# Kernel optimization log

Measured on AMD Instinct MI355X. Metric: run time of the kernel, lower is better.

The kernel has to match this reference:

```python
import jax, jax.numpy as jnp
import numpy as np

DT = 0.001  # fixed dt in SimplifiedSSM.forward
LN_EPS = 1e-5


def _layernorm(x, g, b):
    m = jnp.mean(x, axis=-1, keepdims=True)
    v = jnp.mean(jnp.square(x - m), axis=-1, keepdims=True)
    return (x - m) * jax.lax.rsqrt(v + LN_EPS) * g + b


def setup_inputs() -> dict:
    key = jax.random.key(0)
    ks = jax.random.split(key, 12)
    Bn, C, H, W = 8, 1024, 32, 32
    depth, S = 4, 128
    d = C
    inp = {
        "x": jax.random.normal(ks[0], (Bn, C, H, W), dtype=jnp.float32),
        # SSM params, stacked over depth. A scaled by 0.1 for numerical stability
        # of the length-1024 recurrence (same math, tamer eigenvalues).
        "A": 0.1 * jax.random.normal(ks[1], (depth, S, S), dtype=jnp.float32),
        "Bp": jax.random.normal(ks[2], (depth, S, d), dtype=jnp.float32),
        "Cp": jax.random.normal(ks[3], (depth, d, S), dtype=jnp.float32),
        "Dp": jax.random.normal(ks[4], (depth, d), dtype=jnp.float32),
        # Linear layers (PyTorch convention: y = x @ W.T + b)
        "Wi": jax.random.normal(ks[5], (depth, d, d), dtype=jnp.float32) / np.sqrt(d),
        "bi": jax.random.normal(ks[6], (depth, d), dtype=jnp.float32) * 0.01,
        "Wo": jax.random.normal(ks[7], (depth, d, d), dtype=jnp.float32) / np.sqrt(d),
        "bo": jax.random.normal(ks[8], (depth, d), dtype=jnp.float32) * 0.01,
        # LayerNorm affine params
        "gamma": jnp.ones((depth, d), dtype=jnp.float32),
        "beta": jnp.zeros((depth, d), dtype=jnp.float32),
    }
    return inp


def reference(x, A, Bp, Cp, Dp, Wi, bi, Wo, bo, gamma, beta):
    Bn, C, H, W = x.shape
    depth, S, _ = A.shape
    # b c h w -> b (h w) c
    seq = x.reshape(Bn, C, H * W).transpose(0, 2, 1)
    eye = jnp.eye(S, dtype=x.dtype)
    for i in range(depth):
        n = _layernorm(seq, gamma[i], beta[i])
        u = n @ Wi[i].T + bi[i]                       # (B, L, d)
        A_bar = eye + DT * A[i]                       # (S, S)
        ub = jnp.einsum('bld,sd->lbs', u, DT * Bp[i]) # (L, B, S)

        def step(h, ub_t):
            h = h @ A_bar.T + ub_t
            return h, h

        h0 = jnp.zeros((Bn, S), dtype=x.dtype)
        _, hs = jax.lax.scan(step, h0, ub)            # hs: (L, B, S)
        y = jnp.einsum('lbs,ds->bld', hs, Cp[i]) + u * Dp[i]
        seq = seq + y @ Wo[i].T + bo[i]
    return seq.transpose(0, 2, 1).reshape(Bn, C, H, W)
```

## Files before the change

kernel.cpp:

```cpp
#include <hip/hip_runtime.h>
#include <stdint.h>

#define DT_STEP 0.001f
#define LN_EPS  1e-5f
#define Bn      8
#define Lseq    1024
#define Dm      1024
#define Sn      128
#define DEPTH   4
#define Mrows   (Bn * Lseq)
#define Qc      32
#define NCHUNK  (Lseq / Qc)
#define NPOW    33

typedef short bf16x8 __attribute__((ext_vector_type(8)));
typedef float f32x4  __attribute__((ext_vector_type(4)));

__device__ __forceinline__ unsigned short f2bf(float f) {
    unsigned int u = __float_as_uint(f);
    u += 0x7fffu + ((u >> 16) & 1u);
    return (unsigned short)(u >> 16);
}

#define GLOAD_LDS16(gp, lp)                                                \
    __builtin_amdgcn_global_load_lds(                                      \
        (const __attribute__((address_space(1))) unsigned int*)(gp),       \
        (__attribute__((address_space(3))) unsigned int*)(lp), 16, 0, 0)

__global__ __launch_bounds__(256) void prep_conv(const float* __restrict__ Wo,
                                                 const float* __restrict__ Dp,
                                                 const float* __restrict__ Bp,
                                                 const float* __restrict__ bi,
                                                 const float* __restrict__ bo,
                                                 unsigned short* __restrict__ Woh,
                                                 unsigned short* __restrict__ Wo2h,
                                                 unsigned short* __restrict__ Bph,
                                                 float* __restrict__ c2dt,
                                                 float* __restrict__ boeff) {
    int z = blockIdx.y;
    int bx = blockIdx.x;
    int tid = threadIdx.x;
    if (bx < 1024) {
        int i = (bx * 256 + tid) * 4;
        const float* S = Wo + (size_t)z * Dm * Dm;
        float4 v = *(const float4*)(S + i);
        int c = i & (Dm - 1);
        float4 d = *(const float4*)(Dp + (size_t)z * Dm + c);
        ushort4 o1, o2;
        o1.x = f2bf(v.x); o1.y = f2bf(v.y); o1.z = f2bf(v.z); o1.w = f2bf(v.w);
        o2.x = f2bf(v.x * d.x); o2.y = f2bf(v.y * d.y);
        o2.z = f2bf(v.z * d.z); o2.w = f2bf(v.w * d.w);
        *(ushort4*)(Woh  + (size_t)z * Dm * Dm + i) = o1;
        *(ushort4*)(Wo2h + (size_t)z * Dm * Dm + i) = o2;
        return;
    } else if (bx < 1152) {
        int i = ((bx - 1024) * 256 + tid) * 4;
        float4 v = *(const float4*)(Bp + (size_t)z * Sn * Dm + i);
        ushort4 o;
        o.x = f2bf(v.x); o.y = f2bf(v.y); o.z = f2bf(v.z); o.w = f2bf(v.w);
        *(ushort4*)(Bph + (size_t)z * Sn * Dm + i) = o;
        return;
    }
    int j = bx - 1152;
    float acc;
    if (j < Sn) {
        const float* br = Bp + ((size_t)z * Sn + j) * Dm;
        const float* bb = bi + (size_t)z * Dm;
        float4 v = *(const float4*)(br + tid * 4);
        float4 w = *(const float4*)(bb + tid * 4);
        acc = v.x * w.x + v.y * w.y + v.z * w.z + v.w * w.w;
    } else {
        int c = j - Sn;
        const float* wr = Wo + ((size_t)z * Dm + c) * Dm;
        const float* dp = Dp + (size_t)z * Dm;
        const float* bb = bi + (size_t)z * Dm;
        float4 w = *(const float4*)(wr + tid * 4);
        float4 d = *(const float4*)(dp + tid * 4);
        float4 b = *(const float4*)(bb + tid * 4);
        acc = w.x * d.x * b.x + w.y * d.y * b.y + w.z * d.z * b.z + w.w * d.w * b.w;
    }
#pragma unroll
    for (int off = 32; off > 0; off >>= 1) acc += __shfl_down(acc, off, 64);
    __shared__ float red[4];
    if ((tid & 63) == 0) red[tid >> 6] = acc;
    __syncthreads();
    if (tid == 0) {
        float tot = red[0] + red[1] + red[2] + red[3];
        if (j < Sn) c2dt[z * Sn + j] = DT_STEP * tot;
        else        boeff[(size_t)z * Dm + (j - Sn)] = bo[(size_t)z * Dm + (j - Sn)] + tot;
    }
}

__global__ __launch_bounds__(256) void transpose_pre(const float* __restrict__ Wi,
                                                     unsigned short* __restrict__ WiTh,
                                                     const float* __restrict__ Cp,
                                                     unsigned short* __restrict__ CpTh) {
    __shared__ float t[32][33];
    int z = blockIdx.z;
    const float* S;
    unsigned short* D;
    int R, C, r0, c0;
    if ((int)blockIdx.x < 32) {
        S = Wi + (size_t)z * Dm * Dm;  D = WiTh + (size_t)z * Dm * Dm;
        R = Dm; C = Dm;
        r0 = blockIdx.y * 32; c0 = blockIdx.x * 32;
    } else {
        S = Cp + (size_t)z * Dm * Sn;  D = CpTh + (size_t)z * Dm * Sn;
        R = Dm; C = Sn;
        r0 = blockIdx.y * 32; c0 = (blockIdx.x - 32) * 32;
    }
    int tx = threadIdx.x & 31, ty = threadIdx.x >> 5;
    for (int rr = ty; rr < 32; rr += 8)
        t[rr][tx] = S[(size_t)(r0 + rr) * C + c0 + tx];
    __syncthreads();
    for (int rr = ty; rr < 32; rr += 8)
        D[(size_t)(c0 + rr) * R + r0 + tx] = f2bf(t[tx][rr]);
}

__global__ __launch_bounds__(1024) void transpose_bll(const float* __restrict__ src,
                                                      float* __restrict__ dst) {
    __shared__ float tile[32][33];
    int b  = blockIdx.z;
    int i0 = blockIdx.y * 32, j0 = blockIdx.x * 32;
    int tx = threadIdx.x, ty = threadIdx.y;
    const float* S = src + (size_t)b * Dm * Lseq;
    float*       D = dst + (size_t)b * Dm * Lseq;
    tile[ty][tx] = S[(size_t)(j0 + ty) * 1024 + i0 + tx];
    __syncthreads();
    D[(size_t)(i0 + ty) * 1024 + j0 + tx] = tile[tx][ty];
}

__global__ __launch_bounds__(512) void ln_ub(
    const float* __restrict__ seq,
    unsigned short* __restrict__ nbuf,
    const unsigned short* __restrict__ M2,
    float* __restrict__ ub,
    const float* __restrict__ gam,
    const float* __restrict__ bet,
    const float* __restrict__ c2dtL) {
    __shared__ __align__(16) unsigned short As[256 * 8];
    __shared__ __align__(16) unsigned short Bs[1024 * 8];
    __shared__ float mrow[32], rrow[32];
    int row0 = blockIdx.x * 32;
    int tid = threadIdx.x;

    {
        int r = tid >> 4, l = tid & 15;
        const float* xr = seq + (size_t)(row0 + r) * Dm + l * 4;
        float s = 0.f, ss = 0.f;
#pragma unroll
        for (int j = 0; j < 16; j++) {
            float4 v = *(const float4*)(xr + j * 64);
            s  += v.x + v.y + v.z + v.w;
            ss += v.x * v.x + v.y * v.y + v.z * v.z + v.w * v.w;
        }
        s += __shfl_xor(s, 1, 16);  ss += __shfl_xor(ss, 1, 16);
        s += __shfl_xor(s, 2, 16);  ss += __shfl_xor(ss, 2, 16);
        s += __shfl_xor(s, 4, 16);  ss += __shfl_xor(ss, 4, 16);
        s += __shfl_xor(s, 8, 16);  ss += __shfl_xor(ss, 8, 16);
        if (l == 0) {
            float mean = s / (float)Dm;
            float var  = ss / (float)Dm - mean * mean;
            mrow[r] = mean;
            rrow[r] = rsqrtf(var + LN_EPS);
        }
    }
    __syncthreads();
#pragma unroll
    for (int g = 0; g < 8; g++) {
        int gi = tid + g * 512;
        int rA = gi >> 7, gc = gi & 127;
        int col = gc * 8;
        const float* p = seq + (size_t)(row0 + rA) * Dm + col;
        float4 v0 = *(const float4*)(p);
        float4 v1 = *(const float4*)(p + 4);
        float m = mrow[rA], rs = rrow[rA];
        float4 g0 = *(const float4*)(gam + col);
        float4 g1 = *(const float4*)(gam + col + 4);
        float4 b0 = *(const float4*)(bet + col);
        float4 b1 = *(const float4*)(bet + col + 4);
        bf16x8 pk;
        pk[0] = (short)f2bf((v0.x - m) * rs * g0.x + b0.x);
        pk[1] = (short)f2bf((v0.y - m) * rs * g0.y + b0.y);
        pk[2] = (short)f2bf((v0.z - m) * rs * g0.z + b0.z);
        pk[3] = (short)f2bf((v0.w - m) * rs * g0.w + b0.w);
        pk[4] = (short)f2bf((v1.x - m) * rs * g1.x + b1.x);
        pk[5] = (short)f2bf((v1.y - m) * rs * g1.y + b1.y);
        pk[6] = (short)f2bf((v1.z - m) * rs * g1.z + b1.z);
        pk[7] = (short)f2bf((v1.w - m) * rs * g1.w + b1.w);
        *(bf16x8*)(nbuf + (size_t)(row0 + rA) * Dm + col) = pk;
    }
    __syncthreads();

    int wave = tid >> 6, lane = tid & 63;
    int wn = wave * 16;
    int lr = lane & 15, lq = lane >> 4;

    int rowA = tid >> 3;
    int kclA = (tid & 7) ^ ((tid >> 3) & 7);
    int rowS[2], kclS[2], slotOff[2];
#pragma unroll
    for (int q = 0; q < 2; q++) {
        int s = tid + q * 512;
        rowS[q] = s >> 3;
        kclS[q] = (s & 7) ^ ((s >> 3) & 7);
        slotOff[q] = s * 8;
    }
    int aoff[2][2], boff[2];
#pragma unroll
    for (int i = 0; i < 2; i++)
#pragma unroll
        for (int h = 0; h < 2; h++) {
            int ra = i * 16 + lr;
            aoff[i][h] = (ra * 8 + ((lq + 4 * h) ^ (ra & 7))) * 8;
        }
#pragma unroll
    for (int h = 0; h < 2; h++) {
        int rn = wn + lr;
        boff[h] = (rn * 8 + ((lq + 4 * h) ^ (rn & 7))) * 8;
    }

    f32x4 acc[2];
#pragma unroll
    for (int i = 0; i < 2; i++) acc[i] = (f32x4){0.f, 0.f, 0.f, 0.f};

    for (int k0 = 0; k0 < Dm; k0 += 64) {
        const unsigned short* Abr = nbuf + (size_t)row0 * Dm + k0;
        const unsigned short* Bbr = M2 + k0;
        __syncthreads();
        if (tid < 256)
            GLOAD_LDS16(Abr + (size_t)rowA * Dm + kclA * 8, &As[tid * 8]);
#pragma unroll
        for (int q = 0; q < 2; q++)
            GLOAD_LDS16(Bbr + (size_t)rowS[q] * Dm + kclS[q] * 8, &Bs[slotOff[q]]);
        __syncthreads();
#pragma unroll
        for (int h = 0; h < 2; h++) {
            bf16x8 af[2], bfr;
#pragma unroll
            for (int i = 0; i < 2; i++) af[i] = *(const bf16x8*)&As[aoff[i][h]];
            bfr = *(const bf16x8*)&Bs[boff[h]];
#pragma unroll
            for (int i = 0; i < 2; i++)
                acc[i] = __builtin_amdgcn_mfma_f32_16x16x32_bf16(af[i], bfr,
                                                                 acc[i], 0, 0, 0);
        }
    }
#pragma unroll
    for (int i = 0; i < 2; i++)
#pragma unroll
        for (int r = 0; r < 4; r++) {
            int row = row0 + i * 16 + lq * 4 + r;
            int col = wn + lr;
            ub[(size_t)row * Sn + col] = acc[i][r] + c2dtL[col];
        }
}

__device__ __forceinline__ void gemm64_body(
    int flat, unsigned short* As, unsigned short* Bs,
    const unsigned short* __restrict__ A, const unsigned short* __restrict__ B,
    float* __restrict__ C, const float* __restrict__ bias, int K) {
    int rb = flat & 63, cb = flat >> 6;
    int row0 = rb * 128, col0 = cb * 64;
    int tid  = threadIdx.x;
    int wave = tid >> 6, lane = tid & 63;
    int wm = (wave & 1) * 64, wn = (wave >> 1) * 16;
    int lr = lane & 15, lq = lane >> 4;

    int rowS[2], kclS[2], slotOff[2];
#pragma unroll
    for (int q = 0; q < 2; q++) {
        int s = tid + q * 512;
        rowS[q] = s >> 3;
        kclS[q] = (s & 7) ^ ((s >> 3) & 7);
        slotOff[q] = s * 8;
    }
    int rowB = tid >> 3;
    int kclB = (tid & 7) ^ ((tid >> 3) & 7);

    int aoff[4][2], boff[2];
#pragma unroll
    for (int i = 0; i < 4; i++)
#pragma unroll
        for (int h = 0; h < 2; h++) {
            int ra = wm + i * 16 + lr;
            aoff[i][h] = (ra * 8 + ((lq + 4 * h) ^ (ra & 7))) * 8;
        }
#pragma unroll
    for (int h = 0; h < 2; h++) {
        int rn = wn + lr;
        boff[h] = (rn * 8 + ((lq + 4 * h) ^ (rn & 7))) * 8;
    }

    f32x4 acc[4];
#pragma unroll
    for (int i = 0; i < 4; i++) acc[i] = (f32x4){0.f, 0.f, 0.f, 0.f};

    for (int k0 = 0; k0 < K; k0 += 64) {
        const unsigned short* Abr = A + (size_t)row0 * K + k0;
        const unsigned short* Bbr = B + (size_t)col0 * K + k0;
        __syncthreads();
#pragma unroll
        for (int q = 0; q < 2; q++)
            GLOAD_LDS16(Abr + (size_t)rowS[q] * K + kclS[q] * 8, &As[slotOff[q]]);
        GLOAD_LDS16(Bbr + (size_t)rowB * K + kclB * 8, &Bs[tid * 8]);
        __syncthreads();
#pragma unroll
        for (int h = 0; h < 2; h++) {
            bf16x8 af[4], bf;
#pragma unroll
            for (int i = 0; i < 4; i++) af[i] = *(const bf16x8*)&As[aoff[i][h]];
            bf = *(const bf16x8*)&Bs[boff[h]];
#pragma unroll
            for (int i = 0; i < 4; i++)
                acc[i] = __builtin_amdgcn_mfma_f32_16x16x32_bf16(af[i], bf,
                                                                 acc[i], 0, 0, 0);
        }
    }
#pragma unroll
    for (int i = 0; i < 4; i++)
#pragma unroll
        for (int r = 0; r < 4; r++) {
            int row = row0 + wm + i * 16 + lq * 4 + r;
            int col = col0 + wn + lr;
            size_t idx = (size_t)row * Dm + col;
            float v = acc[i][r];
            if (bias) v += bias[col];
            C[idx] = C[idx] + v;
        }
}

__global__ __launch_bounds__(512) void mega2(
    int mode,
    const unsigned short* __restrict__ nbuf,
    const unsigned short* __restrict__ W4,
    float* __restrict__ seq,
    const float* __restrict__ boeff,
    const float* __restrict__ ub,
    float* __restrict__ hs,
    unsigned short* __restrict__ hs_bf,
    const float* __restrict__ PowL,
    float* __restrict__ carryb) {
    __shared__ __align__(16) char smem[33280];
    int tid = threadIdx.x;
    int bid = blockIdx.x;

    bool isSerial;
    int sid, gflat;
    if (mode == 0)      { isSerial = (bid & 1) == 0; sid = bid >> 1; gflat = bid >> 1; }
    else if (mode == 1) { int q = bid / 33, r = bid % 33;
                          isSerial = (r == 0); sid = q; gflat = 256 + q * 32 + r - 1; }
    else                { int q = bid / 3, r = bid % 3;
                          isSerial = (r == 0); sid = q; gflat = 512 + q * 2 + (r - 1); }

    if (!isSerial) {
        unsigned short* As = (unsigned short*)smem;
        unsigned short* Bs = (unsigned short*)(smem + 16384);
        gemm64_body(gflat, As, Bs, nbuf, W4, seq, boeff, Dm);
        return;
    }

    __builtin_amdgcn_s_setprio(1);

    if (mode == 0) {
        float* hsh = (float*)smem;
        float* hp  = hsh + 128;
        int b = sid >> 5, c = sid & 31;
        int s = tid & 127, kq = tid >> 7;
        const float* Abar = PowL + (size_t)Sn * Sn;
        float arow[32];
#pragma unroll
        for (int j = 0; j < 32; j += 4) {
            float4 v = *(const float4*)(Abar + (size_t)s * Sn + kq * 32 + j);
            arow[j] = v.x; arow[j + 1] = v.y; arow[j + 2] = v.z; arow[j + 3] = v.w;
        }
        if (tid < 128) hsh[tid] = 0.f;
        __syncthreads();
        size_t base = (size_t)(b * Lseq + c * Qc) * Sn + s;
        float ut = (kq == 0) ? ub[base] : 0.f;
        const float* hq = &hsh[kq * 32];
        for (int t = 0; t < Qc; t++) {
            float utn = (kq == 0 && t + 1 < Qc) ? ub[base + (size_t)(t + 1) * Sn] : 0.f;
            float a0 = 0.f, a1 = 0.f, a2 = 0.f, a3 = 0.f;
#pragma unroll
            for (int j = 0; j < 32; j += 16) {
                float4 h0 = *(const float4*)&hq[j];
                float4 h1 = *(const float4*)&hq[j + 4];
                float4 h2 = *(const float4*)&hq[j + 8];
                float4 h3 = *(const float4*)&hq[j + 12];
                a0 += arow[j + 0] * h0.x + arow[j + 1] * h0.y + arow[j + 2] * h0.z + arow[j + 3] * h0.w;
                a1 += arow[j + 4] * h1.x + arow[j + 5] * h1.y + arow[j + 6] * h1.z + arow[j + 7] * h1.w;
                a2 += arow[j + 8] * h2.x + arow[j + 9] * h2.y + arow[j + 10] * h2.z + arow[j + 11] * h2.w;
                a3 += arow[j + 12] * h3.x + arow[j + 13] * h3.y + arow[j + 14] * h3.z + arow[j + 15] * h3.w;
            }
            hp[kq * 128 + s] = (a0 + a1) + (a2 + a3);
            __syncthreads();
            if (kq == 0) {
                float hv = ut + (hp[s] + hp[128 + s]) + (hp[256 + s] + hp[384 + s]);
                hs[base + (size_t)t * Sn] = hv;
                hsh[s] = hv;
            }
            __syncthreads();
            ut = utn;
        }
    } else if (mode == 1) {
        float* csh = (float*)smem;
        float* cp  = csh + 128;
        int b = sid;
        int s = tid & 127, kq = tid >> 7;
        const float* AQ = PowL + (size_t)Qc * Sn * Sn;
        float arow[32];
#pragma unroll
        for (int j = 0; j < 32; j += 4) {
            float4 v = *(const float4*)(AQ + (size_t)s * Sn + kq * 32 + j);
            arow[j] = v.x; arow[j + 1] = v.y; arow[j + 2] = v.z; arow[j + 3] = v.w;
        }
        if (tid < 128) csh[tid] = 0.f;
        __syncthreads();
        float len = (kq == 0) ? hs[(size_t)(b * Lseq + Qc - 1) * Sn + s] : 0.f;
        const float* cq = &csh[kq * 32];
        for (int c = 0; c < NCHUNK; c++) {
            float le_c = len;
            len = (kq == 0 && c + 1 < NCHUNK)
                    ? hs[(size_t)(b * Lseq + (c + 1) * Qc + Qc - 1) * Sn + s] : 0.f;
            if (kq == 0) carryb[((size_t)b * NCHUNK + c) * Sn + s] = csh[s];
            float a0 = 0.f, a1 = 0.f, a2 = 0.f, a3 = 0.f;
#pragma unroll
            for (int j = 0; j < 32; j += 16) {
                float4 h0 = *(const float4*)&cq[j];
                float4 h1 = *(const float4*)&cq[j + 4];
                float4 h2 = *(const float4*)&cq[j + 8];
                float4 h3 = *(const float4*)&cq[j + 12];
                a0 += arow[j + 0] * h0.x + arow[j + 1] * h0.y + arow[j + 2] * h0.z + arow[j + 3] * h0.w;
                a1 += arow[j + 4] * h1.x + arow[j + 5] * h1.y + arow[j + 6] * h1.z + arow[j + 7] * h1.w;
                a2 += arow[j + 8] * h2.x + arow[j + 9] * h2.y + arow[j + 10] * h2.z + arow[j + 11] * h2.w;
                a3 += arow[j + 12] * h3.x + arow[j + 13] * h3.y + arow[j + 14] * h3.z + arow[j + 15] * h3.w;
            }
            cp[kq * 128 + s] = (a0 + a1) + (a2 + a3);
            __syncthreads();
            if (kq == 0)
                csh[s] = le_c + (cp[s] + cp[128 + s]) + (cp[256 + s] + cp[384 + s]);
            __syncthreads();
        }
    } else {
        float* Pl = (float*)smem;
        float* cl = (float*)(smem + 16896);
        int t = sid & 31, c4 = sid >> 5;
        const float* P = PowL + (size_t)(t + 1) * (Sn * Sn);
#pragma unroll
        for (int cc = 0; cc < 4; cc++)
            for (int idx = tid; idx < Bn * Sn; idx += 512)
                cl[cc * 1024 + idx] =
                    carryb[((size_t)(idx >> 7) * NCHUNK + (c4 * 4 + cc)) * Sn + (idx & 127)];
        int s = tid & 127, bh = tid >> 7;
        float acc[4][2];
#pragma unroll
        for (int cc = 0; cc < 4; cc++) { acc[cc][0] = 0.f; acc[cc][1] = 0.f; }
        for (int kh = 0; kh < 4; kh++) {
            __syncthreads();
            for (int idx = tid; idx < Sn * 32; idx += 512) {
                int r = idx >> 5, kk = idx & 31;
                Pl[r * 33 + kk] = P[(size_t)r * Sn + kh * 32 + kk];
            }
            __syncthreads();
            for (int kk = 0; kk < 32; kk++) {
                float pw = Pl[s * 33 + kk];
                int kg = kh * 32 + kk;
#pragma unroll
                for (int cc = 0; cc < 4; cc++)
#pragma unroll
                    for (int j = 0; j < 2; j++)
                        acc[cc][j] += pw * cl[cc * 1024 + (bh * 2 + j) * Sn + kg];
            }
        }
#pragma unroll
        for (int cc = 0; cc < 4; cc++) {
            int c = c4 * 4 + cc;
#pragma unroll
            for (int j = 0; j < 2; j++) {
                int bb = bh * 2 + j;
                size_t rowi = (size_t)(bb * Lseq + c * Qc + t) * Sn + s;
                hs_bf[rowi] = f2bf(hs[rowi] + acc[cc][j]);
            }
        }
    }
    __builtin_amdgcn_s_setprio(0);
}

__global__ __launch_bounds__(512) void gemm_w3k(const unsigned short* __restrict__ hs_bf,
                                                const unsigned short* __restrict__ W3,
                                                float* __restrict__ seq) {
    __shared__ __align__(16) unsigned short As[1024 * 8];
    __shared__ __align__(16) unsigned short Bs[512 * 8];
    gemm64_body(blockIdx.x, As, Bs, hs_bf, W3, seq, nullptr, Sn);
}

__device__ __forceinline__ void gemm128_body(
    int flat, int ny,
    const unsigned short* __restrict__ A, int sA,
    const unsigned short* __restrict__ Bz, int sB,
    unsigned short* __restrict__ C, int N, int K, float scale,
    unsigned short* As, unsigned short* Bs) {
    int rb = flat % ny, cb = flat / ny;
    int row0 = rb * 128, col0 = cb * 128;
    int tid  = threadIdx.x;
    int wave = tid >> 6, lane = tid & 63;
    int wm = (wave & 1) * 64, wn = (wave >> 1) * 32;
    int lr = lane & 15, lq = lane >> 4;

    int rowS[2], kclS[2], slotOff[2];
#pragma unroll
    for (int q = 0; q < 2; q++) {
        int s = tid + q * 512;
        rowS[q] = s >> 3;
        kclS[q] = (s & 7) ^ ((s >> 3) & 7);
        slotOff[q] = s * 8;
    }
    int aoff[4][2], boff[2][2];
#pragma unroll
    for (int i = 0; i < 4; i++)
#pragma unroll
        for (int h = 0; h < 2; h++) {
            int ra = wm + i * 16 + lr;
            aoff[i][h] = (ra * 8 + ((lq + 4 * h) ^ (ra & 7))) * 8;
        }
#pragma unroll
    for (int j = 0; j < 2; j++)
#pragma unroll
        for (int h = 0; h < 2; h++) {
            int rn = wn + j * 16 + lr;
            boff[j][h] = (rn * 8 + ((lq + 4 * h) ^ (rn & 7))) * 8;
        }

    const unsigned short* Bb = Bz + (size_t)col0 * sB;

    f32x4 acc[4][2];
#pragma unroll
    for (int i = 0; i < 4; i++)
#pragma unroll
        for (int j = 0; j < 2; j++) acc[i][j] = (f32x4){0.f, 0.f, 0.f, 0.f};

    for (int k0 = 0; k0 < K; k0 += 64) {
        const unsigned short* Abr = A + (size_t)row0 * sA + k0;
        const unsigned short* Bbr = Bb + k0;
        __syncthreads();
#pragma unroll
        for (int q = 0; q < 2; q++) {
            GLOAD_LDS16(Abr + (size_t)rowS[q] * sA + kclS[q] * 8, &As[slotOff[q]]);
            GLOAD_LDS16(Bbr + (size_t)rowS[q] * sB + kclS[q] * 8, &Bs[slotOff[q]]);
        }
        __syncthreads();
#pragma unroll
        for (int h = 0; h < 2; h++) {
            bf16x8 af[4], bfr[2];
#pragma unroll
            for (int i = 0; i < 4; i++) af[i]  = *(const bf16x8*)&As[aoff[i][h]];
#pragma unroll
            for (int j = 0; j < 2; j++) bfr[j] = *(const bf16x8*)&Bs[boff[j][h]];
#pragma unroll
            for (int i = 0; i < 4; i++)
#pragma unroll
                for (int j = 0; j < 2; j++)
                    acc[i][j] = __builtin_amdgcn_mfma_f32_16x16x32_bf16(af[i], bfr[j],
                                                                       acc[i][j], 0, 0, 0);
        }
    }
#pragma unroll
    for (int i = 0; i < 4; i++)
#pragma unroll
        for (int j = 0; j < 2; j++)
#pragma unroll
            for (int r = 0; r < 4; r++) {
                int row = row0 + wm + i * 16 + lq * 4 + r;
                int col = col0 + wn + j * 16 + lr;
                C[(size_t)row * N + col] = f2bf(acc[i][j][r] * scale);
            }
}

__global__ __launch_bounds__(512) void gemm_pre(
    const unsigned short* __restrict__ Bph,
    const unsigned short* __restrict__ WiTh,
    unsigned short* __restrict__ M2h,
    const unsigned short* __restrict__ Woh,
    const unsigned short* __restrict__ CpTh,
    unsigned short* __restrict__ W3h,
    const unsigned short* __restrict__ Wo2h,
    unsigned short* __restrict__ W4h) {
    __shared__ __align__(16) unsigned short As[1024 * 8];
    __shared__ __align__(16) unsigned short Bs[1024 * 8];
    const long WW = (long)Dm * Dm;
    const long SW = (long)Sn * Dm;
    int bid = blockIdx.x;
    if (bid < 32) {
        int z = bid >> 3, flat = bid & 7;
        gemm128_body(flat, 1, Bph + (size_t)z * SW, Dm, WiTh + (size_t)z * WW, Dm,
                     M2h + (size_t)z * SW, Dm, Dm, DT_STEP, As, Bs);
    } else if (bid < 64) {
        int b2 = bid - 32;
        int z = b2 >> 3, flat = b2 & 7;
        gemm128_body(flat, 8, Woh + (size_t)z * WW, Dm, CpTh + (size_t)z * SW, Dm,
                     W3h + (size_t)z * SW, Sn, Dm, 1.f, As, Bs);
    } else {
        int b3 = bid - 64;
        int z = b3 >> 6, flat = b3 & 63;
        gemm128_body(flat, 8, Wo2h + (size_t)z * WW, Dm, WiTh + (size_t)z * WW, Dm,
                     W4h + (size_t)z * WW, Dm, Dm, 1.f, As, Bs);
    }
}

__global__ __launch_bounds__(128) void pow_init(const float* __restrict__ Amat,
                                                float* __restrict__ Pow) {
    int i = blockIdx.x;
    int s = blockIdx.y;
    int k = threadIdx.x;
    float eye = (s == k) ? 1.f : 0.f;
    size_t base = (size_t)i * NPOW * (Sn * Sn);
    Pow[base + (size_t)s * Sn + k] = eye;
    Pow[base + (size_t)(Sn * Sn) + (size_t)s * Sn + k] =
        eye + DT_STEP * Amat[(size_t)i * Sn * Sn + (size_t)s * Sn + k];
}

__global__ __launch_bounds__(256) void pow_mul(float* __restrict__ Pow, int m, int kmax) {
    int job = blockIdx.z;
    int i  = job / kmax;
    int kk = job % kmax + 1;
    const float* Pa = Pow + ((size_t)i * NPOW + m) * (Sn * Sn);
    const float* Pb = Pow + ((size_t)i * NPOW + kk) * (Sn * Sn);
    float*       Pc = Pow + ((size_t)i * NPOW + m + kk) * (Sn * Sn);
    int r0 = blockIdx.y * 64, c0 = blockIdx.x * 32;
    __shared__ float Asl[64 * 129];
    __shared__ float Bsl[128 * 32];
    int tx = threadIdx.x, ty = threadIdx.y;
    int tid = ty * 16 + tx;
    for (int idx = tid; idx < 64 * 128; idx += 256) {
        int r = idx >> 7, cc = idx & 127;
        Asl[r * 129 + cc] = Pa[(size_t)(r0 + r) * 128 + cc];
    }
    for (int idx = tid; idx < 128 * 32; idx += 256) {
        int r = idx >> 5, cc = idx & 31;
        Bsl[r * 32 + cc] = Pb[(size_t)r * 128 + c0 + cc];
    }
    __syncthreads();
    float acc[4][2] = {{0.f,0.f},{0.f,0.f},{0.f,0.f},{0.f,0.f}};
    for (int k = 0; k < 128; k++) {
        float b0 = Bsl[k * 32 + tx * 2];
        float b1 = Bsl[k * 32 + tx * 2 + 1];
#pragma unroll
        for (int r = 0; r < 4; r++) {
            float a = Asl[(ty * 4 + r) * 129 + k];
            acc[r][0] += a * b0;
            acc[r][1] += a * b1;
        }
    }
#pragma unroll
    for (int r = 0; r < 4; r++) {
        Pc[(size_t)(r0 + ty * 4 + r) * 128 + c0 + tx * 2]     = acc[r][0];
        Pc[(size_t)(r0 + ty * 4 + r) * 128 + c0 + tx * 2 + 1] = acc[r][1];
    }
}

extern "C" void kernel_launch(void* const* d_in, const int* in_sizes, int n_in,
                              void* d_out, int out_size, void* d_ws, size_t ws_size,
                              hipStream_t stream) {
    const float* x     = (const float*)d_in[0];
    const float* Am    = (const float*)d_in[1];
    const float* Bp    = (const float*)d_in[2];
    const float* Cp    = (const float*)d_in[3];
    const float* Dp    = (const float*)d_in[4];
    const float* Wi    = (const float*)d_in[5];
    const float* bi    = (const float*)d_in[6];
    const float* Wo    = (const float*)d_in[7];
    const float* bo    = (const float*)d_in[8];
    const float* gamma = (const float*)d_in[9];
    const float* beta  = (const float*)d_in[10];
    float* out = (float*)d_out;
    (void)in_sizes; (void)n_in; (void)out_size; (void)ws_size;

    char* ws = (char*)d_ws;
    float*          seq   = (float*)(ws + (size_t)0);
    unsigned short* nbuf  = (unsigned short*)(ws + (size_t)33554432);
    unsigned short* WiTh  = (unsigned short*)(ws + (size_t)33554432);
    unsigned short* Woh   = (unsigned short*)(ws + (size_t)41943040);
    unsigned short* W4h   = (unsigned short*)(ws + (size_t)50331648);
    float*          boeff = (float*)(ws + (size_t)58720256);
    float*          ub    = (float*)(ws + (size_t)67108864);
    float*          hs    = (float*)(ws + (size_t)71303168);
    unsigned short* hs_bf = (unsigned short*)(ws + (size_t)75497472);
    float*          Pow   = (float*)(ws + (size_t)77594624);
    float*          carry = (float*)(ws + (size_t)86245376);
    unsigned short* Wo2h  = (unsigned short*)(ws + (size_t)94765056);
    unsigned short* Bph   = (unsigned short*)(ws + (size_t)103153664);
    unsigned short* CpTh  = (unsigned short*)(ws + (size_t)104202240);
    unsigned short* M2h   = (unsigned short*)(ws + (size_t)105250816);
    unsigned short* W3h   = (unsigned short*)(ws + (size_t)106299392);
    float*          c2dt  = (float*)(ws + (size_t)107347968);

    const long SW = (long)Sn * Dm;

    hipLaunchKernelGGL(prep_conv, dim3(2304, DEPTH), dim3(256), 0, stream,
                       Wo, Dp, Bp, bi, bo, Woh, Wo2h, Bph, c2dt, boeff);
    hipLaunchKernelGGL(transpose_pre, dim3(36, 32, DEPTH), dim3(256), 0, stream,
                       Wi, WiTh, Cp, CpTh);

    hipLaunchKernelGGL(gemm_pre, dim3(320), dim3(512), 0, stream,
                       Bph, WiTh, M2h, Woh, CpTh, W3h, Wo2h, W4h);

    hipLaunchKernelGGL(transpose_bll, dim3(32, 32, Bn), dim3(32, 32), 0, stream, x, seq);

    hipLaunchKernelGGL(pow_init, dim3(DEPTH, Sn), dim3(Sn), 0, stream, Am, Pow);
    for (int m = 1; m < Qc; m <<= 1) {
        hipLaunchKernelGGL(pow_mul, dim3(4, 2, DEPTH * m), dim3(16, 16), 0, stream,
                           Pow, m, m);
    }

    for (int i = 0; i < DEPTH; i++) {
        const unsigned short* M2_i = M2h + (size_t)i * SW;
        const unsigned short* W3_i = W3h + (size_t)i * SW;
        const unsigned short* W4_i = W4h + (size_t)i * (size_t)(Dm * Dm);
        const float* PowL = Pow + (size_t)i * NPOW * (Sn * Sn);

        hipLaunchKernelGGL(ln_ub, dim3(256), dim3(512), 0, stream,
                           seq, nbuf, M2_i, ub, gamma + i * Dm, beta + i * Dm,
                           c2dt + i * Sn);
        hipLaunchKernelGGL(mega2, dim3(512), dim3(512), 0, stream,
                           0, nbuf, W4_i, seq, boeff + i * Dm,
                           ub, hs, hs_bf, PowL, carry);
        hipLaunchKernelGGL(mega2, dim3(264), dim3(512), 0, stream,
                           1, nbuf, W4_i, seq, boeff + i * Dm,
                           ub, hs, hs_bf, PowL, carry);
        hipLaunchKernelGGL(mega2, dim3(768), dim3(512), 0, stream,
                           2, nbuf, W4_i, seq, boeff + i * Dm,
                           ub, hs, hs_bf, PowL, carry);
        hipLaunchKernelGGL(gemm_w3k, dim3(1024), dim3(512), 0, stream,
                           hs_bf, W3_i, seq);
    }

    hipLaunchKernelGGL(transpose_bll, dim3(32, 32, Bn), dim3(32, 32), 0, stream, seq, out);
}
```

Baseline: 705.4 us.

## Use 128x128 GEMM tiles for the W4 projection inside mega2 and rebalance blocks

Adds a 128x128-tile bf16 MFMA GEMM body and uses it in place of the 64-row tile for the output projection that runs alongside the serial scan blocks. This halves the number of GEMM tiles and raises operand reuse per loaded byte. The mode 1 and mode 2 block-to-role mappings and grid sizes are reworked to cover the 512 larger tiles, with mode 2 now pairing two serial blocks per GEMM block. The trade-off is fewer, heavier GEMM blocks with more accumulator registers, which could shift how well GEMM work overlaps with the serial recurrence.

```diff
diff --git a/kernel.cpp b/kernel.cpp
--- a/kernel.cpp
+++ b/kernel.cpp
@@ -330,6 +330,87 @@
         }
 }
 
+__device__ __forceinline__ void gemm128r_body(
+    int flat, unsigned short* As, unsigned short* Bs,
+    const unsigned short* __restrict__ A, const unsigned short* __restrict__ B,
+    float* __restrict__ C, const float* __restrict__ bias, int K) {
+    int rb = flat & 63, cb = flat >> 6;
+    int row0 = rb * 128, col0 = cb * 128;
+    int tid  = threadIdx.x;
+    int wave = tid >> 6, lane = tid & 63;
+    int wm = (wave & 1) * 64, wn = (wave >> 1) * 32;
+    int lr = lane & 15, lq = lane >> 4;
+
+    int rowS[2], kclS[2], slotOff[2];
+#pragma unroll
+    for (int q = 0; q < 2; q++) {
+        int s = tid + q * 512;
+        rowS[q] = s >> 3;
+        kclS[q] = (s & 7) ^ ((s >> 3) & 7);
+        slotOff[q] = s * 8;
+    }
+    int aoff[4][2], boff[2][2];
+#pragma unroll
+    for (int i = 0; i < 4; i++)
+#pragma unroll
+        for (int h = 0; h < 2; h++) {
+            int ra = wm + i * 16 + lr;
+            aoff[i][h] = (ra * 8 + ((lq + 4 * h) ^ (ra & 7))) * 8;
+        }
+#pragma unroll
+    for (int j = 0; j < 2; j++)
+#pragma unroll
+        for (int h = 0; h < 2; h++) {
+            int rn = wn + j * 16 + lr;
+            boff[j][h] = (rn * 8 + ((lq + 4 * h) ^ (rn & 7))) * 8;
+        }
+
+    f32x4 acc[4][2];
+#pragma unroll
+    for (int i = 0; i < 4; i++)
+#pragma unroll
+        for (int j = 0; j < 2; j++) acc[i][j] = (f32x4){0.f, 0.f, 0.f, 0.f};
+
+    for (int k0 = 0; k0 < K; k0 += 64) {
+        const unsigned short* Abr = A + (size_t)row0 * K + k0;
+        const unsigned short* Bbr = B + (size_t)col0 * K + k0;
+        __syncthreads();
+#pragma unroll
+        for (int q = 0; q < 2; q++) {
+            GLOAD_LDS16(Abr + (size_t)rowS[q] * K + kclS[q] * 8, &As[slotOff[q]]);
+            GLOAD_LDS16(Bbr + (size_t)rowS[q] * K + kclS[q] * 8, &Bs[slotOff[q]]);
+        }
+        __syncthreads();
+#pragma unroll
+        for (int h = 0; h < 2; h++) {
+            bf16x8 af[4], bfr[2];
+#pragma unroll
+            for (int i = 0; i < 4; i++) af[i]  = *(const bf16x8*)&As[aoff[i][h]];
+#pragma unroll
+            for (int j = 0; j < 2; j++) bfr[j] = *(const bf16x8*)&Bs[boff[j][h]];
+#pragma unroll
+            for (int i = 0; i < 4; i++)
+#pragma unroll
+                for (int j = 0; j < 2; j++)
+                    acc[i][j] = __builtin_amdgcn_mfma_f32_16x16x32_bf16(af[i], bfr[j],
+                                                                       acc[i][j], 0, 0, 0);
+        }
+    }
+#pragma unroll
+    for (int i = 0; i < 4; i++)
+#pragma unroll
+        for (int j = 0; j < 2; j++)
+#pragma unroll
+            for (int r = 0; r < 4; r++) {
+                int row = row0 + wm + i * 16 + lq * 4 + r;
+                int col = col0 + wn + j * 16 + lr;
+                size_t idx = (size_t)row * Dm + col;
+                float v = acc[i][j][r];
+                if (bias) v += bias[col];
+                C[idx] = C[idx] + v;
+            }
+}
+
 __global__ __launch_bounds__(512) void mega2(
     int mode,
     const unsigned short* __restrict__ nbuf,
@@ -348,15 +429,15 @@
     bool isSerial;
     int sid, gflat;
     if (mode == 0)      { isSerial = (bid & 1) == 0; sid = bid >> 1; gflat = bid >> 1; }
-    else if (mode == 1) { int q = bid / 33, r = bid % 33;
-                          isSerial = (r == 0); sid = q; gflat = 256 + q * 32 + r - 1; }
+    else if (mode == 1) { int q = bid / 17, r = bid % 17;
+                          isSerial = (r == 0); sid = q; gflat = 256 + q * 16 + r - 1; }
     else                { int q = bid / 3, r = bid % 3;
-                          isSerial = (r == 0); sid = q; gflat = 512 + q * 2 + (r - 1); }
+                          isSerial = (r < 2); sid = q * 2 + r; gflat = 384 + q; }
 
     if (!isSerial) {
         unsigned short* As = (unsigned short*)smem;
         unsigned short* Bs = (unsigned short*)(smem + 16384);
-        gemm64_body(gflat, As, Bs, nbuf, W4, seq, boeff, Dm);
+        gemm128r_body(gflat, As, Bs, nbuf, W4, seq, boeff, Dm);
         return;
     }
 
@@ -725,10 +806,10 @@
         hipLaunchKernelGGL(mega2, dim3(512), dim3(512), 0, stream,
                            0, nbuf, W4_i, seq, boeff + i * Dm,
                            ub, hs, hs_bf, PowL, carry);
-        hipLaunchKernelGGL(mega2, dim3(264), dim3(512), 0, stream,
+        hipLaunchKernelGGL(mega2, dim3(136), dim3(512), 0, stream,
                            1, nbuf, W4_i, seq, boeff + i * Dm,
                            ub, hs, hs_bf, PowL, carry);
-        hipLaunchKernelGGL(mega2, dim3(768), dim3(512), 0, stream,
+        hipLaunchKernelGGL(mega2, dim3(384), dim3(512), 0, stream,
                            2, nbuf, W4_i, seq, boeff + i * Dm,
                            ub, hs, hs_bf, PowL, carry);
         hipLaunchKernelGGL(gemm_w3k, dim3(1024), dim3(512), 0, stream,
```

New measurement: 719.5 us. About the same (+2.0%).

## Process four SSM chunks per serial block with full-row registers and double-buffered state

Applied to the files above, without the earlier changes.

In mode 0, each serial block now handles four independent chunks, one per 128-thread group. Each thread keeps a full 128-element row of A_bar in registers instead of a 32-element slice of a split-K reduction. The state is double-buffered in shared memory, which removes the partial-sum exchange and one barrier per timestep. The grid is re-partitioned to one serial block per four GEMM blocks (320 blocks). The risk is much higher register pressure from the 128-float array, which could cause spills or lower occupancy, and the four-times-longer dot product per thread lengthens each step's critical path.

```diff
diff --git a/kernel.cpp b/kernel.cpp
--- a/kernel.cpp
+++ b/kernel.cpp
@@ -347,7 +347,8 @@
 
     bool isSerial;
     int sid, gflat;
-    if (mode == 0)      { isSerial = (bid & 1) == 0; sid = bid >> 1; gflat = bid >> 1; }
+    if (mode == 0)      { int q = bid / 5, r = bid % 5;
+                          isSerial = (r == 0); sid = q; gflat = q * 4 + (r - 1); }
     else if (mode == 1) { int q = bid / 33, r = bid % 33;
                           isSerial = (r == 0); sid = q; gflat = 256 + q * 32 + r - 1; }
     else                { int q = bid / 3, r = bid % 3;
@@ -363,44 +364,44 @@
     __builtin_amdgcn_s_setprio(1);
 
     if (mode == 0) {
-        float* hsh = (float*)smem;
-        float* hp  = hsh + 128;
-        int b = sid >> 5, c = sid & 31;
-        int s = tid & 127, kq = tid >> 7;
+        float* bufA = (float*)smem;
+        float* bufB = bufA + 512;
+        int cc = tid >> 7, s = tid & 127;
+        int chunk = sid * 4 + cc;
+        int b = chunk >> 5, c = chunk & 31;
         const float* Abar = PowL + (size_t)Sn * Sn;
-        float arow[32];
-#pragma unroll
-        for (int j = 0; j < 32; j += 4) {
-            float4 v = *(const float4*)(Abar + (size_t)s * Sn + kq * 32 + j);
-            arow[j] = v.x; arow[j + 1] = v.y; arow[j + 2] = v.z; arow[j + 3] = v.w;
-        }
-        if (tid < 128) hsh[tid] = 0.f;
+        float arow[Sn];
+#pragma unroll
+        for (int k = 0; k < Sn; k += 4) {
+            float4 v = *(const float4*)(Abar + (size_t)s * Sn + k);
+            arow[k] = v.x; arow[k + 1] = v.y; arow[k + 2] = v.z; arow[k + 3] = v.w;
+        }
+        bufA[cc * 128 + s] = 0.f;
         __syncthreads();
         size_t base = (size_t)(b * Lseq + c * Qc) * Sn + s;
-        float ut = (kq == 0) ? ub[base] : 0.f;
-        const float* hq = &hsh[kq * 32];
+        float ut = ub[base];
+        float* cur = bufA;
+        float* nxt = bufB;
         for (int t = 0; t < Qc; t++) {
-            float utn = (kq == 0 && t + 1 < Qc) ? ub[base + (size_t)(t + 1) * Sn] : 0.f;
+            float utn = (t + 1 < Qc) ? ub[base + (size_t)(t + 1) * Sn] : 0.f;
+            const float* hch = cur + cc * 128;
             float a0 = 0.f, a1 = 0.f, a2 = 0.f, a3 = 0.f;
 #pragma unroll
-            for (int j = 0; j < 32; j += 16) {
-                float4 h0 = *(const float4*)&hq[j];
-                float4 h1 = *(const float4*)&hq[j + 4];
-                float4 h2 = *(const float4*)&hq[j + 8];
-                float4 h3 = *(const float4*)&hq[j + 12];
-                a0 += arow[j + 0] * h0.x + arow[j + 1] * h0.y + arow[j + 2] * h0.z + arow[j + 3] * h0.w;
-                a1 += arow[j + 4] * h1.x + arow[j + 5] * h1.y + arow[j + 6] * h1.z + arow[j + 7] * h1.w;
-                a2 += arow[j + 8] * h2.x + arow[j + 9] * h2.y + arow[j + 10] * h2.z + arow[j + 11] * h2.w;
-                a3 += arow[j + 12] * h3.x + arow[j + 13] * h3.y + arow[j + 14] * h3.z + arow[j + 15] * h3.w;
+            for (int k = 0; k < Sn; k += 16) {
+                float4 h0 = *(const float4*)&hch[k];
+                float4 h1 = *(const float4*)&hch[k + 4];
+                float4 h2 = *(const float4*)&hch[k + 8];
+                float4 h3 = *(const float4*)&hch[k + 12];
+                a0 += arow[k + 0] * h0.x + arow[k + 1] * h0.y + arow[k + 2] * h0.z + arow[k + 3] * h0.w;
+                a1 += arow[k + 4] * h1.x + arow[k + 5] * h1.y + arow[k + 6] * h1.z + arow[k + 7] * h1.w;
+                a2 += arow[k + 8] * h2.x + arow[k + 9] * h2.y + arow[k + 10] * h2.z + arow[k + 11] * h2.w;
+                a3 += arow[k + 12] * h3.x + arow[k + 13] * h3.y + arow[k + 14] * h3.z + arow[k + 15] * h3.w;
             }
-            hp[kq * 128 + s] = (a0 + a1) + (a2 + a3);
+            float hv = ut + (a0 + a1) + (a2 + a3);
+            hs[base + (size_t)t * Sn] = hv;
+            nxt[cc * 128 + s] = hv;
             __syncthreads();
-            if (kq == 0) {
-                float hv = ut + (hp[s] + hp[128 + s]) + (hp[256 + s] + hp[384 + s]);
-                hs[base + (size_t)t * Sn] = hv;
-                hsh[s] = hv;
-            }
-            __syncthreads();
+            float* tmp = cur; cur = nxt; nxt = tmp;
             ut = utn;
         }
     } else if (mode == 1) {
@@ -722,7 +723,7 @@
         hipLaunchKernelGGL(ln_ub, dim3(256), dim3(512), 0, stream,
                            seq, nbuf, M2_i, ub, gamma + i * Dm, beta + i * Dm,
                            c2dt + i * Sn);
-        hipLaunchKernelGGL(mega2, dim3(512), dim3(512), 0, stream,
+        hipLaunchKernelGGL(mega2, dim3(320), dim3(512), 0, stream,
                            0, nbuf, W4_i, seq, boeff + i * Dm,
                            ub, hs, hs_bf, PowL, carry);
         hipLaunchKernelGGL(mega2, dim3(264), dim3(512), 0, stream,
```

Measured after the change: 878.0 us. 24.5% more time.
